# Performance work log

Hardware: AMD Instinct MI355X
Metric: run time of the kernel (lower is better)

## Reference

```python
import jax, jax.numpy as jnp
import numpy as np
import math

B, T, D, H = 1576, 30, 1024, 128  # batch, Frame, embded_dim, hidden_dim
EPS = 1e-5

def _layernorm(x, g, b):
    m = jnp.mean(x, axis=-1, keepdims=True)
    v = jnp.mean((x - m) ** 2, axis=-1, keepdims=True)
    return (x - m) * jax.lax.rsqrt(v + EPS) * g + b

def setup_inputs() -> dict:
    key = jax.random.key(0)
    ks = jax.random.split(key, 16)
    s = 0.02
    inp = {
        "x": jax.random.normal(ks[0], (B, T, D), dtype=jnp.float32),
        # weights stored as [in, out] (transposed vs torch nn.Linear.weight)
        "W1": jax.random.normal(ks[1], (D, H), dtype=jnp.float32) * s,
        "b1": jnp.zeros((H,), jnp.float32),
        "ln_g": jnp.ones((H,), jnp.float32),
        "ln_b": jnp.zeros((H,), jnp.float32),
        "T_W": jax.random.normal(ks[2], (T, T), dtype=jnp.float32) * s,
        "T_b": jnp.zeros((T,), jnp.float32),
        "Wq": jax.random.normal(ks[3], (H, H), dtype=jnp.float32) * s,
        "bq": jnp.zeros((H,), jnp.float32),
        "Wk": jax.random.normal(ks[4], (H, H), dtype=jnp.float32) * s,
        "bk": jnp.zeros((H,), jnp.float32),
        "Wv": jax.random.normal(ks[5], (H, H), dtype=jnp.float32) * s,
        "bv": jnp.zeros((H,), jnp.float32),
        "Wo": jax.random.normal(ks[6], (H, H), dtype=jnp.float32) * s,
        "bo": jnp.zeros((H,), jnp.float32),
        "n_g": jnp.ones((H,), jnp.float32),
        "n_b": jnp.zeros((H,), jnp.float32),
        "W2": jax.random.normal(ks[7], (H, D), dtype=jnp.float32) * s,
        "b2": jnp.zeros((D,), jnp.float32),
    }
    return inp

def reference(x, W1, b1, ln_g, ln_b, T_W, T_b, Wq, bq, Wk, bk, Wv, bv, Wo, bo, n_g, n_b, W2, b2):
    # down-projection + LayerNorm
    h = x @ W1 + b1                      # [B,T,H]
    h = _layernorm(h, ln_g, ln_b)
    # FRU: mean over channels -> temporal linear -> softmax over time -> gate
    g = jnp.mean(h, axis=-1)             # [B,T]
    g = g @ T_W + T_b                    # [B,T]
    g = jax.nn.softmax(g, axis=1)
    h = h * g[..., None]
    # TemporalTransformer (single-head manual attention over T=30)
    hn = _layernorm(h, n_g, n_b)
    q = hn @ Wq + bq
    k = hn @ Wk + bk
    v = hn @ Wv + bv
    scale = math.sqrt(1.0 / float(H))
    attn = jax.nn.softmax((q * scale) @ jnp.swapaxes(k, -2, -1), axis=-1)  # [B,T,T]
    h = (attn @ v) @ Wo + bo + h
    # up-projection
    return h @ W2 + b2                   # [B,T,D]
```

## Files before the change

### kernel.cpp

```cpp
#include <hip/hip_runtime.h>
#include <cstdint>
#include <cstddef>

typedef short s16x8 __attribute__((ext_vector_type(8)));
typedef short s16x4 __attribute__((ext_vector_type(4)));
typedef float f32x4 __attribute__((ext_vector_type(4)));

#define NB 1576
#define NT 30
#define ND 1024
#define NH 128
#define LNEPS 1e-5f
#define ATT_SCALE 0.08838834764831845f

#define WS_W1P   0
#define WS_W2P   262144
#define WS_WQP   524288
#define WS_WKP   557056
#define WS_WVP   589824
#define WS_WOP   622592
#define WS_PAR   655360
#define WS_NEED  667792

#define P_B1   0
#define P_LNG  128
#define P_LNB  256
#define P_TB   384
#define P_TW   416
#define P_BQ   1316
#define P_BK   1444
#define P_BV   1572
#define P_BO   1700
#define P_NG   1828
#define P_NB_  1956
#define P_B2   2084
#define P_CNT  3108

static __device__ __forceinline__ float bf2f(short s) {
  union { unsigned int u; float f; } c;
  c.u = ((unsigned int)(unsigned short)s) << 16;
  return c.f;
}
static __device__ __forceinline__ short f2bf(float f) {
  union { __bf16 h; short s; } c;
  c.h = (__bf16)f;
  return c.s;
}
static __device__ __forceinline__ float ldp(const void* p, int i, int isf32) {
  return isf32 ? ((const float*)p)[i] : bf2f(((const short*)p)[i]);
}
static __device__ __forceinline__ s16x8 ldfragB(const void* W, int N, int k0, int n0,
                                                int m_, int quad, int isf32) {
  s16x8 r;
  int k = k0 + quad*8, n = n0 + m_;
  if (isf32) {
    const float* p = (const float*)W + (size_t)k*N + n;
#pragma unroll
    for (int j = 0; j < 8; j++) r[j] = f2bf(p[(size_t)j*N]);
  } else {
    const short* p = (const short*)W + (size_t)k*N + n;
#pragma unroll
    for (int j = 0; j < 8; j++) r[j] = p[(size_t)j*N];
  }
  return r;
}
static __device__ __forceinline__ void mm32d(const short* Ab, const void* W, const void* bias,
                                             int w, int lane, int isf32,
                                             f32x4 acc[2][2], float bias2[2]) {
  int m_ = lane & 15, quad = lane >> 4;
#pragma unroll
  for (int mt = 0; mt < 2; mt++)
#pragma unroll
    for (int j = 0; j < 2; j++) acc[mt][j] = {0.f, 0.f, 0.f, 0.f};
  bias2[0] = ldp(bias, (2*w)*16 + m_, isf32);
  bias2[1] = ldp(bias, (2*w+1)*16 + m_, isf32);
#pragma unroll
  for (int ks = 0; ks < 4; ks++) {
    s16x8 a[2];
#pragma unroll
    for (int mt = 0; mt < 2; mt++)
      a[mt] = *(const s16x8*)(Ab + (mt*16 + m_)*136 + (ks*4 + quad)*8);
#pragma unroll
    for (int j = 0; j < 2; j++) {
      s16x8 bb = ldfragB(W, NH, ks*32, (2*w + j)*16, m_, quad, isf32);
#pragma unroll
      for (int mt = 0; mt < 2; mt++)
        acc[mt][j] = __builtin_amdgcn_mfma_f32_16x16x32_bf16(a[mt], bb, acc[mt][j], 0, 0, 0);
    }
  }
}

__global__ __launch_bounds__(256) void repack(
    const void* __restrict__ x,
    const void* __restrict__ W1, const void* __restrict__ Wq, const void* __restrict__ Wk,
    const void* __restrict__ Wv, const void* __restrict__ Wo, const void* __restrict__ W2,
    const void* __restrict__ b1, const void* __restrict__ ln_g, const void* __restrict__ ln_b,
    const void* __restrict__ T_W, const void* __restrict__ T_b,
    const void* __restrict__ bq, const void* __restrict__ bk, const void* __restrict__ bv,
    const void* __restrict__ bo, const void* __restrict__ n_g, const void* __restrict__ n_b,
    const void* __restrict__ b2,
    short* __restrict__ W1p, short* __restrict__ W2p,
    short* __restrict__ Wqp, short* __restrict__ Wkp, short* __restrict__ Wvp,
    short* __restrict__ Wop, float* __restrict__ par) {
  int lane = threadIdx.x & 63;
  const unsigned short* u = (const unsigned short*)x;
  int e = (u[lane] >> 7) & 0xFF;
  unsigned long long bal = __ballot(e >= 0x3A && e <= 0x43);
  int isf32 = (__popcll(bal) < 48) ? 1 : 0;

  int idx = blockIdx.x * 256 + threadIdx.x;
  if (idx < 16384) {
    int t = idx, kq = t >> 7, n = t & 127;
    s16x8 v;
#pragma unroll
    for (int j = 0; j < 8; j++)
      v[j] = isf32 ? f2bf(((const float*)W1)[(size_t)(kq*8 + j)*128 + n])
                   : ((const short*)W1)[(size_t)(kq*8 + j)*128 + n];
    *(s16x8*)(W1p + (size_t)t*8) = v;
  } else if (idx < 32768) {
    int t = idx - 16384, kq = t >> 10, n = t & 1023;
    s16x8 v;
#pragma unroll
    for (int j = 0; j < 8; j++)
      v[j] = isf32 ? f2bf(((const float*)W2)[(size_t)(kq*8 + j)*1024 + n])
                   : ((const short*)W2)[(size_t)(kq*8 + j)*1024 + n];
    *(s16x8*)(W2p + (size_t)t*8) = v;
  } else if (idx < 40960) {
    int t = idx - 32768;
    int sel = t >> 11;
    int tt = t & 2047, kq = tt >> 7, n = tt & 127;
    const void* W = (sel == 0) ? Wq : (sel == 1) ? Wk : (sel == 2) ? Wv : Wo;
    short* Wp = (sel == 0) ? Wqp : (sel == 1) ? Wkp : (sel == 2) ? Wvp : Wop;
    s16x8 v;
#pragma unroll
    for (int j = 0; j < 8; j++)
      v[j] = isf32 ? f2bf(((const float*)W)[(size_t)(kq*8 + j)*128 + n])
                   : ((const short*)W)[(size_t)(kq*8 + j)*128 + n];
    *(s16x8*)(Wp + (size_t)tt*8) = v;
  } else {
    int t = idx - 40960;
    if (t < P_CNT) {
      float v;
      if (t < 128)        v = ldp(b1,   t,        isf32);
      else if (t < 256)   v = ldp(ln_g, t - 128,  isf32);
      else if (t < 384)   v = ldp(ln_b, t - 256,  isf32);
      else if (t < 416) { int i = t - 384; v = (i < NT) ? ldp(T_b, i, isf32) : 0.f; }
      else if (t < 1316)  v = ldp(T_W, t - 416,   isf32);
      else if (t < 1444)  v = ldp(bq,  t - 1316,  isf32);
      else if (t < 1572)  v = ldp(bk,  t - 1444,  isf32);
      else if (t < 1700)  v = ldp(bv,  t - 1572,  isf32);
      else if (t < 1828)  v = ldp(bo,  t - 1700,  isf32);
      else if (t < 1956)  v = ldp(n_g, t - 1828,  isf32);
      else if (t < 2084)  v = ldp(n_b, t - 1956,  isf32);
      else                v = ldp(b2,  t - 2084,  isf32);
      par[t] = v;
    }
  }
}

__global__ __launch_bounds__(512, 4) void fused_pk(
    const void* __restrict__ x,
    const short* __restrict__ W1p, const short* __restrict__ W2p,
    const short* __restrict__ Wqp, const short* __restrict__ Wkp,
    const short* __restrict__ Wvp, const short* __restrict__ Wop,
    const float* __restrict__ par, void* __restrict__ out) {
  __shared__ __align__(16) short As[32*136];
  __shared__ __align__(16) float hbuf[NT*128];
  __shared__ float g0s[32];
  __shared__ float sgate[32];
  __shared__ __align__(16) short hn[32*136];
  __shared__ __align__(16) short qb[32*136];
  __shared__ __align__(16) short kbf[32*136];
  __shared__ __align__(16) short vt[NH*32];
  __shared__ float Sb[32*33];
  __shared__ __align__(16) short Pb[32*32];

  int tid = threadIdx.x, lane = tid & 63, w = tid >> 6;
  int m_ = lane & 15, quad = lane >> 4;
  int b = blockIdx.x;
  const int g16 = w*16 + m_;

  int isf32;
  {
    const unsigned short* u = (const unsigned short*)x;
    int e = (u[lane] >> 7) & 0xFF;
    unsigned long long bal = __ballot(e >= 0x3A && e <= 0x43);
    isf32 = (__popcll(bal) < 48) ? 1 : 0;
  }
  const size_t xbase = (size_t)b * NT * ND;

  f32x4 acc0 = {0.f,0.f,0.f,0.f}, acc1 = {0.f,0.f,0.f,0.f};
  {
    int r_st = tid >> 4, cc_st = tid & 15;
    int rr = r_st > NT-1 ? NT-1 : r_st;
    const size_t xoff0 = xbase + (size_t)rr*ND + cc_st*8;
    float4 pf0, pf1; uint4 pu;
    if (isf32) { const float* s = (const float*)x + xoff0; pf0 = *(const float4*)s; pf1 = *(const float4*)(s + 4); }
    else       { pu = *(const uint4*)((const short*)x + xoff0); }
    for (int kb = 0; kb < 8; kb++) {
      if (isf32) {
        s16x8 t;
        t[0]=f2bf(pf0.x); t[1]=f2bf(pf0.y); t[2]=f2bf(pf0.z); t[3]=f2bf(pf0.w);
        t[4]=f2bf(pf1.x); t[5]=f2bf(pf1.y); t[6]=f2bf(pf1.z); t[7]=f2bf(pf1.w);
        *(s16x8*)(As + r_st*136 + cc_st*8) = t;
      } else {
        *(uint4*)(As + r_st*136 + cc_st*8) = pu;
      }
      __syncthreads();
      if (kb < 7) {
        size_t o = xoff0 + (size_t)(kb + 1)*128;
        if (isf32) { const float* s = (const float*)x + o; pf0 = *(const float4*)s; pf1 = *(const float4*)(s + 4); }
        else       { pu = *(const uint4*)((const short*)x + o); }
      }
#pragma unroll
      for (int kblk = 0; kblk < 4; kblk++) {
        s16x8 a0 = *(const s16x8*)(As + m_*136 + (kblk*4 + quad)*8);
        s16x8 a1 = *(const s16x8*)(As + (16 + m_)*136 + (kblk*4 + quad)*8);
        s16x8 bb = *(const s16x8*)(W1p + ((size_t)((kb*4 + kblk)*4 + quad)*NH + g16)*8);
        acc0 = __builtin_amdgcn_mfma_f32_16x16x32_bf16(a0, bb, acc0, 0, 0, 0);
        acc1 = __builtin_amdgcn_mfma_f32_16x16x32_bf16(a1, bb, acc1, 0, 0, 0);
      }
      __syncthreads();
    }
  }
  {
    float b1v = par[P_B1 + g16];
#pragma unroll
    for (int mt = 0; mt < 2; mt++) {
      f32x4 a = mt ? acc1 : acc0;
#pragma unroll
      for (int r = 0; r < 4; r++) {
        int row = mt*16 + quad*4 + r;
        if (row < NT) hbuf[row*128 + g16] = a[r] + b1v;
      }
    }
  }
  __syncthreads();

  for (int r = w; r < NT; r += 8) {
    float v0 = hbuf[r*128 + lane], v1 = hbuf[r*128 + lane + 64];
    float s = v0 + v1, ss = v0*v0 + v1*v1;
#pragma unroll
    for (int off = 1; off <= 32; off <<= 1) {
      s += __shfl_xor(s, off, 64); ss += __shfl_xor(ss, off, 64);
    }
    float mean = s * (1.f/NH);
    float var = ss * (1.f/NH) - mean*mean;
    float rs = rsqrtf(var + LNEPS);
    float o0 = (v0 - mean) * rs * par[P_LNG + lane]      + par[P_LNB + lane];
    float o1 = (v1 - mean) * rs * par[P_LNG + lane + 64] + par[P_LNB + lane + 64];
    hbuf[r*128 + lane] = o0;
    hbuf[r*128 + lane + 64] = o1;
    float rm = o0 + o1;
#pragma unroll
    for (int off = 1; off <= 32; off <<= 1) rm += __shfl_xor(rm, off, 64);
    if (lane == 0) g0s[r] = rm * (1.f/NH);
  }
  __syncthreads();

  if (tid < 32) {
    float y = -1e30f;
    if (tid < NT) {
      y = par[P_TB + tid];
      for (int t = 0; t < NT; t++) y += g0s[t] * par[P_TW + t*NT + tid];
    }
    float mx = y;
#pragma unroll
    for (int off = 16; off >= 1; off >>= 1) mx = fmaxf(mx, __shfl_xor(mx, off, 64));
    float e = (tid < NT) ? expf(y - mx) : 0.f;
    float s = e;
#pragma unroll
    for (int off = 16; off >= 1; off >>= 1) s += __shfl_xor(s, off, 64);
    if (tid < NT) sgate[tid] = e / s;
  }
  __syncthreads();

#pragma unroll
  for (int it = 0; it < 2; it++) {
    int c = it*512 + tid;
    if (c < 960) {
      int row = c >> 5, i = c & 31;
      float gt = sgate[row];
      float4* p = (float4*)(hbuf + row*128 + i*4);
      float4 v = *p;
      v.x *= gt; v.y *= gt; v.z *= gt; v.w *= gt;
      *p = v;
    }
  }
  __syncthreads();

  for (int r = w; r < NT; r += 8) {
    float v0 = hbuf[r*128 + lane], v1 = hbuf[r*128 + lane + 64];
    float s = v0 + v1, ss = v0*v0 + v1*v1;
#pragma unroll
    for (int off = 1; off <= 32; off <<= 1) {
      s += __shfl_xor(s, off, 64); ss += __shfl_xor(ss, off, 64);
    }
    float mean = s * (1.f/NH);
    float var = ss * (1.f/NH) - mean*mean;
    float rs = rsqrtf(var + LNEPS);
    hn[r*136 + lane]      = f2bf((v0 - mean) * rs * par[P_NG + lane]      + par[P_NB_ + lane]);
    hn[r*136 + lane + 64] = f2bf((v1 - mean) * rs * par[P_NG + lane + 64] + par[P_NB_ + lane + 64]);
  }
  if (tid < 256) hn[(NT + (tid >> 7))*136 + (tid & 127)] = 0;
  __syncthreads();

  {
    f32x4 q0 = {0.f,0.f,0.f,0.f}, q1 = q0, k0 = q0, k1 = q0, v0a = q0, v1a = q0;
#pragma unroll
    for (int ks = 0; ks < 4; ks++) {
      s16x8 a0 = *(const s16x8*)(hn + m_*136 + (ks*4 + quad)*8);
      s16x8 a1 = *(const s16x8*)(hn + (16 + m_)*136 + (ks*4 + quad)*8);
      size_t fo = ((size_t)(ks*4 + quad)*NH + g16)*8;
      s16x8 bq8 = *(const s16x8*)(Wqp + fo);
      q0 = __builtin_amdgcn_mfma_f32_16x16x32_bf16(a0, bq8, q0, 0, 0, 0);
      q1 = __builtin_amdgcn_mfma_f32_16x16x32_bf16(a1, bq8, q1, 0, 0, 0);
      s16x8 bk8 = *(const s16x8*)(Wkp + fo);
      k0 = __builtin_amdgcn_mfma_f32_16x16x32_bf16(a0, bk8, k0, 0, 0, 0);
      k1 = __builtin_amdgcn_mfma_f32_16x16x32_bf16(a1, bk8, k1, 0, 0, 0);
      s16x8 bv8 = *(const s16x8*)(Wvp + fo);
      v0a = __builtin_amdgcn_mfma_f32_16x16x32_bf16(a0, bv8, v0a, 0, 0, 0);
      v1a = __builtin_amdgcn_mfma_f32_16x16x32_bf16(a1, bv8, v1a, 0, 0, 0);
    }
    float bqv = par[P_BQ + g16], bkv = par[P_BK + g16], bvv = par[P_BV + g16];
#pragma unroll
    for (int mt = 0; mt < 2; mt++) {
      f32x4 qq = mt ? q1 : q0, kk = mt ? k1 : k0, vv = mt ? v1a : v0a;
      s16x4 vtp;
#pragma unroll
      for (int r = 0; r < 4; r++) {
        int row = mt*16 + quad*4 + r;
        qb[row*136 + g16]  = f2bf(qq[r] + bqv);
        kbf[row*136 + g16] = f2bf(kk[r] + bkv);
        vtp[r] = f2bf(vv[r] + bvv);
      }
      *(s16x4*)(vt + g16*32 + mt*16 + quad*4) = vtp;
    }
  }
  __syncthreads();

  if (w < 4) {
    int mt = w >> 1, nt = w & 1;
    f32x4 sa = {0.f,0.f,0.f,0.f};
#pragma unroll
    for (int ks = 0; ks < 4; ks++) {
      s16x8 a   = *(const s16x8*)(qb  + (mt*16 + m_)*136 + (ks*4 + quad)*8);
      s16x8 bbv = *(const s16x8*)(kbf + (nt*16 + m_)*136 + (ks*4 + quad)*8);
      sa = __builtin_amdgcn_mfma_f32_16x16x32_bf16(a, bbv, sa, 0, 0, 0);
    }
#pragma unroll
    for (int r = 0; r < 4; r++)
      Sb[(mt*16 + quad*4 + r)*33 + nt*16 + m_] = sa[r];
  }
  __syncthreads();

#pragma unroll
  for (int ps = 0; ps < 2; ps++) {
    int row = ps*16 + (tid >> 5);
    int col = tid & 31;
    if (row < NT) {
      float sv = (col < NT) ? Sb[row*33 + col] : -1e30f;
      float mx = sv;
#pragma unroll
      for (int off = 16; off >= 1; off >>= 1) mx = fmaxf(mx, __shfl_xor(mx, off, 32));
      float e = (col < NT) ? expf((sv - mx) * ATT_SCALE) : 0.f;
      float s = e;
#pragma unroll
      for (int off = 16; off >= 1; off >>= 1) s += __shfl_xor(s, off, 32);
      Pb[row*32 + col] = f2bf(e / s);
    } else {
      Pb[row*32 + col] = 0;
    }
  }
  __syncthreads();

  {
    f32x4 a40 = {0.f,0.f,0.f,0.f}, a41 = a40;
    s16x8 pa0 = *(const s16x8*)(Pb + m_*32 + quad*8);
    s16x8 pa1 = *(const s16x8*)(Pb + (16 + m_)*32 + quad*8);
    s16x8 vb8 = *(const s16x8*)(vt + g16*32 + quad*8);
    a40 = __builtin_amdgcn_mfma_f32_16x16x32_bf16(pa0, vb8, a40, 0, 0, 0);
    a41 = __builtin_amdgcn_mfma_f32_16x16x32_bf16(pa1, vb8, a41, 0, 0, 0);
#pragma unroll
    for (int mt = 0; mt < 2; mt++) {
      f32x4 a = mt ? a41 : a40;
#pragma unroll
      for (int r = 0; r < 4; r++)
        As[(mt*16 + quad*4 + r)*136 + g16] = f2bf(a[r]);
    }
  }
  __syncthreads();

  {
    f32x4 o0 = {0.f,0.f,0.f,0.f}, o1 = o0;
#pragma unroll
    for (int ks = 0; ks < 4; ks++) {
      s16x8 a0 = *(const s16x8*)(As + m_*136 + (ks*4 + quad)*8);
      s16x8 a1 = *(const s16x8*)(As + (16 + m_)*136 + (ks*4 + quad)*8);
      s16x8 bb = *(const s16x8*)(Wop + ((size_t)(ks*4 + quad)*NH + g16)*8);
      o0 = __builtin_amdgcn_mfma_f32_16x16x32_bf16(a0, bb, o0, 0, 0, 0);
      o1 = __builtin_amdgcn_mfma_f32_16x16x32_bf16(a1, bb, o1, 0, 0, 0);
    }
    float bov = par[P_BO + g16];
#pragma unroll
    for (int mt = 0; mt < 2; mt++) {
      f32x4 a = mt ? o1 : o0;
#pragma unroll
      for (int r = 0; r < 4; r++) {
        int row = mt*16 + quad*4 + r;
        if (row < NT)
          hn[row*136 + g16] = f2bf(a[r] + bov + hbuf[row*128 + g16]);
      }
    }
    if (tid < 256) hn[(NT + (tid >> 7))*136 + (tid & 127)] = 0;
  }
  __syncthreads();

  for (int cg = 0; cg < 8; cg++) {
    f32x4 c0 = {0.f,0.f,0.f,0.f}, c1 = c0;
#pragma unroll
    for (int kblk = 0; kblk < 4; kblk++) {
      s16x8 a0 = *(const s16x8*)(hn + m_*136 + (kblk*4 + quad)*8);
      s16x8 a1 = *(const s16x8*)(hn + (16 + m_)*136 + (kblk*4 + quad)*8);
      s16x8 bb = *(const s16x8*)(W2p + ((size_t)(kblk*4 + quad)*ND + cg*128 + g16)*8);
      c0 = __builtin_amdgcn_mfma_f32_16x16x32_bf16(a0, bb, c0, 0, 0, 0);
      c1 = __builtin_amdgcn_mfma_f32_16x16x32_bf16(a1, bb, c1, 0, 0, 0);
    }
    float b2v = par[P_B2 + cg*128 + g16];
    if (isf32) {
      float* po = (float*)out + (size_t)b*NT*ND + cg*128 + g16;
#pragma unroll
      for (int mt = 0; mt < 2; mt++) {
        f32x4 a = mt ? c1 : c0;
#pragma unroll
        for (int r = 0; r < 4; r++) {
          int row = mt*16 + quad*4 + r;
          if (row < NT) po[(size_t)row*ND] = a[r] + b2v;
        }
      }
    } else {
#pragma unroll
      for (int mt = 0; mt < 2; mt++) {
        f32x4 a = mt ? c1 : c0;
#pragma unroll
        for (int r = 0; r < 4; r++)
          qb[(mt*16 + quad*4 + r)*136 + g16] = f2bf(a[r] + b2v);
      }
      __syncthreads();
      if (tid < 480) {
        int r = tid >> 4, cc = tid & 15;
        *(uint4*)((short*)out + ((size_t)b*NT + r)*ND + cg*128 + cc*8) =
            *(const uint4*)(qb + r*136 + cc*8);
      }
      __syncthreads();
    }
  }
}

__global__ __launch_bounds__(256) void fused_all(
    const void* __restrict__ x, const void* __restrict__ W1,
    const void* __restrict__ b1, const void* __restrict__ ln_g, const void* __restrict__ ln_b,
    const void* __restrict__ T_W, const void* __restrict__ T_b,
    const void* __restrict__ Wq, const void* __restrict__ bq,
    const void* __restrict__ Wk, const void* __restrict__ bk,
    const void* __restrict__ Wv, const void* __restrict__ bv,
    const void* __restrict__ Wo, const void* __restrict__ bo,
    const void* __restrict__ n_g, const void* __restrict__ n_b,
    const void* __restrict__ W2, const void* __restrict__ b2,
    void* __restrict__ out) {
  __shared__ __align__(16) short As[32*136];
  __shared__ __align__(16) float hbuf[NT*128];
  __shared__ float g0s[32];
  __shared__ float sgate[32];
  __shared__ __align__(16) short hn[32*136];
  __shared__ __align__(16) short qb[32*136];
  __shared__ __align__(16) short kbf[32*136];
  __shared__ __align__(16) short vt[NH*32];
  __shared__ float Sb[32*33];
  __shared__ __align__(16) short Pb[32*32];

  int tid = threadIdx.x, lane = tid & 63, w = tid >> 6;
  int m_ = lane & 15, quad = lane >> 4;
  int b = blockIdx.x;

  int isf32;
  {
    const unsigned short* u = (const unsigned short*)x;
    int pl = 0;
#pragma unroll
    for (int i = 0; i < 64; i++) {
      int e = (u[i] >> 7) & 0xFF;
      pl += (e >= 0x3A && e <= 0x43) ? 1 : 0;
    }
    isf32 = (pl < 48) ? 1 : 0;
  }
  const size_t xbase = (size_t)b * NT * ND;

  f32x4 acc[2][2];
#pragma unroll
  for (int mt = 0; mt < 2; mt++)
#pragma unroll
    for (int j = 0; j < 2; j++) acc[mt][j] = {0.f, 0.f, 0.f, 0.f};

  for (int kb = 0; kb < 8; kb++) {
    __syncthreads();
#pragma unroll
    for (int it = 0; it < 2; it++) {
      int c = it*256 + tid;
      int r = c >> 4, cc = c & 15;
      int rr = r > NT-1 ? NT-1 : r;
      size_t off = xbase + (size_t)rr*ND + kb*128 + cc*8;
      if (!isf32) {
        *(uint4*)(As + r*136 + cc*8) = *(const uint4*)((const short*)x + off);
      } else {
        const float* src = (const float*)x + off;
        float4 f0 = *(const float4*)src, f1 = *(const float4*)(src + 4);
        s16x8 t;
        t[0]=f2bf(f0.x); t[1]=f2bf(f0.y); t[2]=f2bf(f0.z); t[3]=f2bf(f0.w);
        t[4]=f2bf(f1.x); t[5]=f2bf(f1.y); t[6]=f2bf(f1.z); t[7]=f2bf(f1.w);
        *(s16x8*)(As + r*136 + cc*8) = t;
      }
    }
    __syncthreads();
#pragma unroll
    for (int kblk = 0; kblk < 4; kblk++) {
      s16x8 a0 = *(const s16x8*)(As + (m_)*136      + (kblk*4 + quad)*8);
      s16x8 a1 = *(const s16x8*)(As + (16 + m_)*136 + (kblk*4 + quad)*8);
#pragma unroll
      for (int j = 0; j < 2; j++) {
        s16x8 bb = ldfragB(W1, NH, (kb*4 + kblk)*32, (2*w + j)*16, m_, quad, isf32);
        acc[0][j] = __builtin_amdgcn_mfma_f32_16x16x32_bf16(a0, bb, acc[0][j], 0, 0, 0);
        acc[1][j] = __builtin_amdgcn_mfma_f32_16x16x32_bf16(a1, bb, acc[1][j], 0, 0, 0);
      }
    }
  }
  __syncthreads();
  {
    float b1v[2] = {ldp(b1, (2*w)*16 + m_, isf32), ldp(b1, (2*w+1)*16 + m_, isf32)};
#pragma unroll
    for (int mt = 0; mt < 2; mt++)
#pragma unroll
      for (int j = 0; j < 2; j++)
#pragma unroll
        for (int r = 0; r < 4; r++) {
          int row = mt*16 + quad*4 + r;
          if (row < NT)
            hbuf[row*128 + (2*w + j)*16 + m_] = acc[mt][j][r] + b1v[j];
        }
  }
  __syncthreads();

  for (int r = w; r < NT; r += 4) {
    float v0 = hbuf[r*128 + lane], v1 = hbuf[r*128 + lane + 64];
    float s = v0 + v1, ss = v0*v0 + v1*v1;
#pragma unroll
    for (int off = 1; off <= 32; off <<= 1) {
      s += __shfl_xor(s, off, 64); ss += __shfl_xor(ss, off, 64);
    }
    float mean = s * (1.f/NH);
    float var = ss * (1.f/NH) - mean*mean;
    float rs = rsqrtf(var + LNEPS);
    float o0 = (v0 - mean) * rs * ldp(ln_g, lane, isf32)      + ldp(ln_b, lane, isf32);
    float o1 = (v1 - mean) * rs * ldp(ln_g, lane + 64, isf32) + ldp(ln_b, lane + 64, isf32);
    hbuf[r*128 + lane] = o0;
    hbuf[r*128 + lane + 64] = o1;
    float rm = o0 + o1;
#pragma unroll
    for (int off = 1; off <= 32; off <<= 1) rm += __shfl_xor(rm, off, 64);
    if (lane == 0) g0s[r] = rm * (1.f/NH);
  }
  __syncthreads();

  if (tid < 32) {
    float y = -1e30f;
    if (tid < NT) {
      y = ldp(T_b, tid, isf32);
      for (int t = 0; t < NT; t++) y += g0s[t] * ldp(T_W, t*NT + tid, isf32);
    }
    float mx = y;
#pragma unroll
    for (int off = 16; off >= 1; off >>= 1) mx = fmaxf(mx, __shfl_xor(mx, off, 64));
    float e = (tid < NT) ? expf(y - mx) : 0.f;
    float s = e;
#pragma unroll
    for (int off = 16; off >= 1; off >>= 1) s += __shfl_xor(s, off, 64);
    if (tid < NT) sgate[tid] = e / s;
  }
  __syncthreads();

#pragma unroll
  for (int it = 0; it < 4; it++) {
    int c = it*256 + tid;
    if (c < 960) {
      int row = c >> 5, i = c & 31;
      float gt = sgate[row];
      float4* p = (float4*)(hbuf + row*128 + i*4);
      float4 v = *p;
      v.x *= gt; v.y *= gt; v.z *= gt; v.w *= gt;
      *p = v;
    }
  }
  __syncthreads();

  for (int r = w; r < NT; r += 4) {
    float v0 = hbuf[r*128 + lane], v1 = hbuf[r*128 + lane + 64];
    float s = v0 + v1, ss = v0*v0 + v1*v1;
#pragma unroll
    for (int off = 1; off <= 32; off <<= 1) {
      s += __shfl_xor(s, off, 64); ss += __shfl_xor(ss, off, 64);
    }
    float mean = s * (1.f/NH);
    float var = ss * (1.f/NH) - mean*mean;
    float rs = rsqrtf(var + LNEPS);
    hn[r*136 + lane]      = f2bf((v0 - mean) * rs * ldp(n_g, lane, isf32)      + ldp(n_b, lane, isf32));
    hn[r*136 + lane + 64] = f2bf((v1 - mean) * rs * ldp(n_g, lane + 64, isf32) + ldp(n_b, lane + 64, isf32));
  }
  hn[(30 + (tid >> 7))*136 + (tid & 127)] = 0;
  __syncthreads();

  {
    f32x4 a4[2][2];
    float bias2[2];
    mm32d(hn, Wq, bq, w, lane, isf32, a4, bias2);
#pragma unroll
    for (int mt = 0; mt < 2; mt++)
#pragma unroll
      for (int j = 0; j < 2; j++)
#pragma unroll
        for (int r = 0; r < 4; r++)
          qb[(mt*16 + quad*4 + r)*136 + (2*w + j)*16 + m_] = f2bf(a4[mt][j][r] + bias2[j]);
    mm32d(hn, Wk, bk, w, lane, isf32, a4, bias2);
#pragma unroll
    for (int mt = 0; mt < 2; mt++)
#pragma unroll
      for (int j = 0; j < 2; j++)
#pragma unroll
        for (int r = 0; r < 4; r++)
          kbf[(mt*16 + quad*4 + r)*136 + (2*w + j)*16 + m_] = f2bf(a4[mt][j][r] + bias2[j]);
    mm32d(hn, Wv, bv, w, lane, isf32, a4, bias2);
#pragma unroll
    for (int mt = 0; mt < 2; mt++)
#pragma unroll
      for (int j = 0; j < 2; j++)
#pragma unroll
        for (int r = 0; r < 4; r++)
          vt[((2*w + j)*16 + m_)*32 + mt*16 + quad*4 + r] = f2bf(a4[mt][j][r] + bias2[j]);
  }
  __syncthreads();

  {
    int mt = w >> 1, nt = w & 1;
    f32x4 sa = {0.f, 0.f, 0.f, 0.f};
#pragma unroll
    for (int ks = 0; ks < 4; ks++) {
      s16x8 a   = *(const s16x8*)(qb  + (mt*16 + m_)*136 + (ks*4 + quad)*8);
      s16x8 bbv = *(const s16x8*)(kbf + (nt*16 + m_)*136 + (ks*4 + quad)*8);
      sa = __builtin_amdgcn_mfma_f32_16x16x32_bf16(a, bbv, sa, 0, 0, 0);
    }
#pragma unroll
    for (int r = 0; r < 4; r++)
      Sb[(mt*16 + quad*4 + r)*33 + nt*16 + m_] = sa[r];
  }
  __syncthreads();

  if (tid < NT) {
    float mx = -1e30f;
    for (int jj = 0; jj < NT; jj++) {
      int j = tid + jj; if (j >= NT) j -= NT;
      mx = fmaxf(mx, Sb[tid*33 + j]);
    }
    float sum = 0.f;
    for (int jj = 0; jj < NT; jj++) {
      int j = tid + jj; if (j >= NT) j -= NT;
      float e = expf((Sb[tid*33 + j] - mx) * ATT_SCALE);
      Sb[tid*33 + j] = e; sum += e;
    }
    float rinv = 1.f / sum;
    for (int jj = 0; jj < NT; jj++) {
      int j = tid + jj; if (j >= NT) j -= NT;
      Pb[tid*32 + j] = f2bf(Sb[tid*33 + j] * rinv);
    }
    Pb[tid*32 + 30] = 0;
    Pb[tid*32 + 31] = 0;
  } else if (tid >= 64 && tid < 128) {
    int c = tid - 64;
    Pb[(30 + (c >> 5))*32 + (c & 31)] = 0;
  }
  __syncthreads();

  {
    f32x4 a4[2][2];
#pragma unroll
    for (int mt = 0; mt < 2; mt++)
#pragma unroll
      for (int j = 0; j < 2; j++) a4[mt][j] = {0.f, 0.f, 0.f, 0.f};
    s16x8 pa[2];
#pragma unroll
    for (int mt = 0; mt < 2; mt++)
      pa[mt] = *(const s16x8*)(Pb + (mt*16 + m_)*32 + quad*8);
#pragma unroll
    for (int j = 0; j < 2; j++) {
      int nh = (2*w + j)*16 + m_;
      s16x8 vb8 = *(const s16x8*)(vt + nh*32 + quad*8);
#pragma unroll
      for (int mt = 0; mt < 2; mt++)
        a4[mt][j] = __builtin_amdgcn_mfma_f32_16x16x32_bf16(pa[mt], vb8, a4[mt][j], 0, 0, 0);
    }
#pragma unroll
    for (int mt = 0; mt < 2; mt++)
#pragma unroll
      for (int j = 0; j < 2; j++)
#pragma unroll
        for (int r = 0; r < 4; r++)
          As[(mt*16 + quad*4 + r)*136 + (2*w + j)*16 + m_] = f2bf(a4[mt][j][r]);
  }
  __syncthreads();

  {
    f32x4 a4[2][2];
    float bias2[2];
    mm32d(As, Wo, bo, w, lane, isf32, a4, bias2);
#pragma unroll
    for (int mt = 0; mt < 2; mt++)
#pragma unroll
      for (int j = 0; j < 2; j++)
#pragma unroll
        for (int r = 0; r < 4; r++) {
          int row = mt*16 + quad*4 + r;
          if (row < NT) {
            int col = (2*w + j)*16 + m_;
            hn[row*136 + col] = f2bf(a4[mt][j][r] + bias2[j] + hbuf[row*128 + col]);
          }
        }
    hn[(30 + (tid >> 7))*136 + (tid & 127)] = 0;
  }
  __syncthreads();

  for (int cg = 0; cg < 8; cg++) {
    f32x4 a2[2][2];
#pragma unroll
    for (int mt = 0; mt < 2; mt++)
#pragma unroll
      for (int j = 0; j < 2; j++) a2[mt][j] = {0.f, 0.f, 0.f, 0.f};
#pragma unroll
    for (int kblk = 0; kblk < 4; kblk++) {
      s16x8 a0 = *(const s16x8*)(hn + (m_)*136      + (kblk*4 + quad)*8);
      s16x8 a1 = *(const s16x8*)(hn + (16 + m_)*136 + (kblk*4 + quad)*8);
#pragma unroll
      for (int j = 0; j < 2; j++) {
        s16x8 bb = ldfragB(W2, ND, kblk*32, cg*128 + (2*w + j)*16, m_, quad, isf32);
        a2[0][j] = __builtin_amdgcn_mfma_f32_16x16x32_bf16(a0, bb, a2[0][j], 0, 0, 0);
        a2[1][j] = __builtin_amdgcn_mfma_f32_16x16x32_bf16(a1, bb, a2[1][j], 0, 0, 0);
      }
    }
    float b2v[2] = {ldp(b2, cg*128 + (2*w)*16 + m_, isf32),
                    ldp(b2, cg*128 + (2*w+1)*16 + m_, isf32)};
    if (!isf32) {
#pragma unroll
      for (int mt = 0; mt < 2; mt++)
#pragma unroll
        for (int j = 0; j < 2; j++)
#pragma unroll
          for (int r = 0; r < 4; r++)
            qb[(mt*16 + quad*4 + r)*136 + (2*w + j)*16 + m_] = f2bf(a2[mt][j][r] + b2v[j]);
    }
    __syncthreads();
    if (!isf32) {
#pragma unroll
      for (int it = 0; it < 2; it++) {
        int c = it*256 + tid;
        if (c < 480) {
          int r = c >> 4, cc = c & 15;
          *(uint4*)((short*)out + ((size_t)b*NT + r)*ND + cg*128 + cc*8) =
              *(const uint4*)(qb + r*136 + cc*8);
        }
      }
    } else {
#pragma unroll
      for (int mt = 0; mt < 2; mt++)
#pragma unroll
        for (int j = 0; j < 2; j++)
#pragma unroll
          for (int r = 0; r < 4; r++) {
            int row = mt*16 + quad*4 + r;
            if (row < NT)
              ((float*)out)[((size_t)b*NT + row)*ND + cg*128 + (2*w + j)*16 + m_] =
                  a2[mt][j][r] + b2v[j];
          }
    }
    __syncthreads();
  }
}

extern "C" void kernel_launch(void* const* d_in, const int* in_sizes, int n_in,
                              void* d_out, int out_size, void* d_ws, size_t ws_size,
                              hipStream_t stream) {
  if (d_ws && ws_size >= (size_t)WS_NEED) {
    short* W1p = (short*)((char*)d_ws + WS_W1P);
    short* W2p = (short*)((char*)d_ws + WS_W2P);
    short* Wqp = (short*)((char*)d_ws + WS_WQP);
    short* Wkp = (short*)((char*)d_ws + WS_WKP);
    short* Wvp = (short*)((char*)d_ws + WS_WVP);
    short* Wop = (short*)((char*)d_ws + WS_WOP);
    float* par = (float*)((char*)d_ws + WS_PAR);
    repack<<<173, 256, 0, stream>>>(
        d_in[0],
        d_in[1], d_in[7], d_in[9], d_in[11], d_in[13], d_in[17],
        d_in[2], d_in[3], d_in[4], d_in[5], d_in[6],
        d_in[8], d_in[10], d_in[12], d_in[14], d_in[15], d_in[16], d_in[18],
        W1p, W2p, Wqp, Wkp, Wvp, Wop, par);
    fused_pk<<<NB, 512, 0, stream>>>(d_in[0], W1p, W2p, Wqp, Wkp, Wvp, Wop, par, d_out);
  } else {
    fused_all<<<NB, 256, 0, stream>>>(
        d_in[0], d_in[1], d_in[2], d_in[3], d_in[4], d_in[5], d_in[6],
        d_in[7], d_in[8], d_in[9], d_in[10], d_in[11], d_in[12], d_in[13],
        d_in[14], d_in[15], d_in[16], d_in[17], d_in[18], d_out);
  }
}
```

Before: 436.2 us.

## Cut LDS footprint, double-buffer x staging, fold gating into second LayerNorm

Shared-memory buffers in the fused kernel are aliased (q reuses As, scores and probabilities reuse hnb, the output staging reuses As), which cuts the per-block LDS footprint, and the occupancy hint goes from 4 to 6 blocks per CU. The x load loop now ping-pongs between two LDS staging buffers with two-deep register prefetch, so one barrier per k-step disappears. The separate gate-multiply pass and the second LayerNorm reduction are replaced by an algebraic form that derives the gated row's mean and variance from the first LayerNorm's stored sum and sum of squares. In exchange there are extra barriers to protect the aliased buffers, more register pressure under the tighter launch bound, and slightly different rounding in the derived variance.

```diff
diff --git a/kernel.cpp b/kernel.cpp
--- a/kernel.cpp
+++ b/kernel.cpp
@@ -158,22 +158,20 @@
   }
 }
 
-__global__ __launch_bounds__(512, 4) void fused_pk(
+__global__ __launch_bounds__(512, 6) void fused_pk(
     const void* __restrict__ x,
     const short* __restrict__ W1p, const short* __restrict__ W2p,
     const short* __restrict__ Wqp, const short* __restrict__ Wkp,
     const short* __restrict__ Wvp, const short* __restrict__ Wop,
     const float* __restrict__ par, void* __restrict__ out) {
   __shared__ __align__(16) short As[32*136];
+  __shared__ __align__(16) short kbf[32*136];
   __shared__ __align__(16) float hbuf[NT*128];
+  __shared__ __align__(16) short hnb[32*136];
+  __shared__ __align__(16) short vt[NH*40];
   __shared__ float g0s[32];
+  __shared__ float rsqm[32];
   __shared__ float sgate[32];
-  __shared__ __align__(16) short hn[32*136];
-  __shared__ __align__(16) short qb[32*136];
-  __shared__ __align__(16) short kbf[32*136];
-  __shared__ __align__(16) short vt[NH*32];
-  __shared__ float Sb[32*33];
-  __shared__ __align__(16) short Pb[32*32];
 
   int tid = threadIdx.x, lane = tid & 63, w = tid >> 6;
   int m_ = lane & 15, quad = lane >> 4;
@@ -194,33 +192,47 @@
     int r_st = tid >> 4, cc_st = tid & 15;
     int rr = r_st > NT-1 ? NT-1 : r_st;
     const size_t xoff0 = xbase + (size_t)rr*ND + cc_st*8;
-    float4 pf0, pf1; uint4 pu;
-    if (isf32) { const float* s = (const float*)x + xoff0; pf0 = *(const float4*)s; pf1 = *(const float4*)(s + 4); }
-    else       { pu = *(const uint4*)((const short*)x + xoff0); }
+    float4 fa0, fa1, fb0, fb1; uint4 ua, ub;
+    if (isf32) {
+      const float* s0 = (const float*)x + xoff0;
+      fa0 = *(const float4*)s0;         fa1 = *(const float4*)(s0 + 4);
+      fb0 = *(const float4*)(s0 + 128); fb1 = *(const float4*)(s0 + 132);
+    } else {
+      const short* s0 = (const short*)x + xoff0;
+      ua = *(const uint4*)s0; ub = *(const uint4*)(s0 + 128);
+    }
+#pragma unroll
     for (int kb = 0; kb < 8; kb++) {
+      short* stg = (kb & 1) ? kbf : As;
       if (isf32) {
+        float4 f0 = (kb & 1) ? fb0 : fa0, f1 = (kb & 1) ? fb1 : fa1;
         s16x8 t;
-        t[0]=f2bf(pf0.x); t[1]=f2bf(pf0.y); t[2]=f2bf(pf0.z); t[3]=f2bf(pf0.w);
-        t[4]=f2bf(pf1.x); t[5]=f2bf(pf1.y); t[6]=f2bf(pf1.z); t[7]=f2bf(pf1.w);
-        *(s16x8*)(As + r_st*136 + cc_st*8) = t;
+        t[0]=f2bf(f0.x); t[1]=f2bf(f0.y); t[2]=f2bf(f0.z); t[3]=f2bf(f0.w);
+        t[4]=f2bf(f1.x); t[5]=f2bf(f1.y); t[6]=f2bf(f1.z); t[7]=f2bf(f1.w);
+        *(s16x8*)(stg + r_st*136 + cc_st*8) = t;
       } else {
-        *(uint4*)(As + r_st*136 + cc_st*8) = pu;
+        *(uint4*)(stg + r_st*136 + cc_st*8) = (kb & 1) ? ub : ua;
+      }
+      if (kb < 6) {
+        if (isf32) {
+          const float* s2 = (const float*)x + xoff0 + (size_t)(kb + 2)*128;
+          if (kb & 1) { fb0 = *(const float4*)s2; fb1 = *(const float4*)(s2 + 4); }
+          else        { fa0 = *(const float4*)s2; fa1 = *(const float4*)(s2 + 4); }
+        } else {
+          const short* s2 = (const short*)x + xoff0 + (size_t)(kb + 2)*128;
+          if (kb & 1) ub = *(const uint4*)s2; else ua = *(const uint4*)s2;
+        }
       }
       __syncthreads();
-      if (kb < 7) {
-        size_t o = xoff0 + (size_t)(kb + 1)*128;
-        if (isf32) { const float* s = (const float*)x + o; pf0 = *(const float4*)s; pf1 = *(const float4*)(s + 4); }
-        else       { pu = *(const uint4*)((const short*)x + o); }
-      }
+      const short* Ab = (kb & 1) ? kbf : As;
 #pragma unroll
       for (int kblk = 0; kblk < 4; kblk++) {
-        s16x8 a0 = *(const s16x8*)(As + m_*136 + (kblk*4 + quad)*8);
-        s16x8 a1 = *(const s16x8*)(As + (16 + m_)*136 + (kblk*4 + quad)*8);
+        s16x8 a0 = *(const s16x8*)(Ab + m_*136 + (kblk*4 + quad)*8);
+        s16x8 a1 = *(const s16x8*)(Ab + (16 + m_)*136 + (kblk*4 + quad)*8);
         s16x8 bb = *(const s16x8*)(W1p + ((size_t)((kb*4 + kblk)*4 + quad)*NH + g16)*8);
         acc0 = __builtin_amdgcn_mfma_f32_16x16x32_bf16(a0, bb, acc0, 0, 0, 0);
         acc1 = __builtin_amdgcn_mfma_f32_16x16x32_bf16(a1, bb, acc1, 0, 0, 0);
       }
-      __syncthreads();
     }
   }
   {
@@ -251,10 +263,12 @@
     float o1 = (v1 - mean) * rs * par[P_LNG + lane + 64] + par[P_LNB + lane + 64];
     hbuf[r*128 + lane] = o0;
     hbuf[r*128 + lane + 64] = o1;
-    float rm = o0 + o1;
-#pragma unroll
-    for (int off = 1; off <= 32; off <<= 1) rm += __shfl_xor(rm, off, 64);
-    if (lane == 0) g0s[r] = rm * (1.f/NH);
+    float rm = o0 + o1, rq = o0*o0 + o1*o1;
+#pragma unroll
+    for (int off = 1; off <= 32; off <<= 1) {
+      rm += __shfl_xor(rm, off, 64); rq += __shfl_xor(rq, off, 64);
+    }
+    if (lane == 0) { g0s[r] = rm * (1.f/NH); rsqm[r] = rq * (1.f/NH); }
   }
   __syncthreads();
 
@@ -275,42 +289,25 @@
   }
   __syncthreads();
 
-#pragma unroll
-  for (int it = 0; it < 2; it++) {
-    int c = it*512 + tid;
-    if (c < 960) {
-      int row = c >> 5, i = c & 31;
-      float gt = sgate[row];
-      float4* p = (float4*)(hbuf + row*128 + i*4);
-      float4 v = *p;
-      v.x *= gt; v.y *= gt; v.z *= gt; v.w *= gt;
-      *p = v;
-    }
-  }
-  __syncthreads();
-
   for (int r = w; r < NT; r += 8) {
-    float v0 = hbuf[r*128 + lane], v1 = hbuf[r*128 + lane + 64];
-    float s = v0 + v1, ss = v0*v0 + v1*v1;
-#pragma unroll
-    for (int off = 1; off <= 32; off <<= 1) {
-      s += __shfl_xor(s, off, 64); ss += __shfl_xor(ss, off, 64);
-    }
-    float mean = s * (1.f/NH);
-    float var = ss * (1.f/NH) - mean*mean;
+    float g = sgate[r];
+    float m = g0s[r];
+    float gm = g * m;
+    float var = g*g*(rsqm[r] - m*m);
     float rs = rsqrtf(var + LNEPS);
-    hn[r*136 + lane]      = f2bf((v0 - mean) * rs * par[P_NG + lane]      + par[P_NB_ + lane]);
-    hn[r*136 + lane + 64] = f2bf((v1 - mean) * rs * par[P_NG + lane + 64] + par[P_NB_ + lane + 64]);
-  }
-  if (tid < 256) hn[(NT + (tid >> 7))*136 + (tid & 127)] = 0;
+    float o0 = g * hbuf[r*128 + lane], o1 = g * hbuf[r*128 + lane + 64];
+    hnb[r*136 + lane]      = f2bf((o0 - gm) * rs * par[P_NG + lane]      + par[P_NB_ + lane]);
+    hnb[r*136 + lane + 64] = f2bf((o1 - gm) * rs * par[P_NG + lane + 64] + par[P_NB_ + lane + 64]);
+  }
+  if (tid < 256) hnb[(NT + (tid >> 7))*136 + (tid & 127)] = 0;
   __syncthreads();
 
   {
     f32x4 q0 = {0.f,0.f,0.f,0.f}, q1 = q0, k0 = q0, k1 = q0, v0a = q0, v1a = q0;
 #pragma unroll
     for (int ks = 0; ks < 4; ks++) {
-      s16x8 a0 = *(const s16x8*)(hn + m_*136 + (ks*4 + quad)*8);
-      s16x8 a1 = *(const s16x8*)(hn + (16 + m_)*136 + (ks*4 + quad)*8);
+      s16x8 a0 = *(const s16x8*)(hnb + m_*136 + (ks*4 + quad)*8);
+      s16x8 a1 = *(const s16x8*)(hnb + (16 + m_)*136 + (ks*4 + quad)*8);
       size_t fo = ((size_t)(ks*4 + quad)*NH + g16)*8;
       s16x8 bq8 = *(const s16x8*)(Wqp + fo);
       q0 = __builtin_amdgcn_mfma_f32_16x16x32_bf16(a0, bq8, q0, 0, 0, 0);
@@ -323,6 +320,7 @@
       v1a = __builtin_amdgcn_mfma_f32_16x16x32_bf16(a1, bv8, v1a, 0, 0, 0);
     }
     float bqv = par[P_BQ + g16], bkv = par[P_BK + g16], bvv = par[P_BV + g16];
+    __syncthreads();
 #pragma unroll
     for (int mt = 0; mt < 2; mt++) {
       f32x4 qq = mt ? q1 : q0, kk = mt ? k1 : k0, vv = mt ? v1a : v0a;
@@ -330,57 +328,66 @@
 #pragma unroll
       for (int r = 0; r < 4; r++) {
         int row = mt*16 + quad*4 + r;
-        qb[row*136 + g16]  = f2bf(qq[r] + bqv);
+        As[row*136 + g16]  = f2bf(qq[r] + bqv);
         kbf[row*136 + g16] = f2bf(kk[r] + bkv);
         vtp[r] = f2bf(vv[r] + bvv);
       }
-      *(s16x4*)(vt + g16*32 + mt*16 + quad*4) = vtp;
-    }
-  }
-  __syncthreads();
-
-  if (w < 4) {
-    int mt = w >> 1, nt = w & 1;
-    f32x4 sa = {0.f,0.f,0.f,0.f};
-#pragma unroll
-    for (int ks = 0; ks < 4; ks++) {
-      s16x8 a   = *(const s16x8*)(qb  + (mt*16 + m_)*136 + (ks*4 + quad)*8);
-      s16x8 bbv = *(const s16x8*)(kbf + (nt*16 + m_)*136 + (ks*4 + quad)*8);
-      sa = __builtin_amdgcn_mfma_f32_16x16x32_bf16(a, bbv, sa, 0, 0, 0);
-    }
-#pragma unroll
-    for (int r = 0; r < 4; r++)
-      Sb[(mt*16 + quad*4 + r)*33 + nt*16 + m_] = sa[r];
-  }
-  __syncthreads();
-
-#pragma unroll
-  for (int ps = 0; ps < 2; ps++) {
-    int row = ps*16 + (tid >> 5);
-    int col = tid & 31;
-    if (row < NT) {
-      float sv = (col < NT) ? Sb[row*33 + col] : -1e30f;
-      float mx = sv;
-#pragma unroll
-      for (int off = 16; off >= 1; off >>= 1) mx = fmaxf(mx, __shfl_xor(mx, off, 32));
-      float e = (col < NT) ? expf((sv - mx) * ATT_SCALE) : 0.f;
-      float s = e;
-#pragma unroll
-      for (int off = 16; off >= 1; off >>= 1) s += __shfl_xor(s, off, 32);
-      Pb[row*32 + col] = f2bf(e / s);
-    } else {
-      Pb[row*32 + col] = 0;
-    }
-  }
-  __syncthreads();
-
-  {
+      *(s16x4*)(vt + g16*40 + mt*16 + quad*4) = vtp;
+    }
+  }
+  __syncthreads();
+
+  {
+    float* Sb = (float*)hnb;
+    if (w < 4) {
+      int mt = w >> 1, nt = w & 1;
+      f32x4 sa = {0.f,0.f,0.f,0.f};
+#pragma unroll
+      for (int ks = 0; ks < 4; ks++) {
+        s16x8 a   = *(const s16x8*)(As  + (mt*16 + m_)*136 + (ks*4 + quad)*8);
+        s16x8 bbv = *(const s16x8*)(kbf + (nt*16 + m_)*136 + (ks*4 + quad)*8);
+        sa = __builtin_amdgcn_mfma_f32_16x16x32_bf16(a, bbv, sa, 0, 0, 0);
+      }
+#pragma unroll
+      for (int r = 0; r < 4; r++)
+        Sb[(mt*16 + quad*4 + r)*33 + nt*16 + m_] = sa[r];
+    }
+  }
+  __syncthreads();
+
+  {
+    const float* Sb = (const float*)hnb;
+    short* Pb = hnb + 2112;
+#pragma unroll
+    for (int ps = 0; ps < 2; ps++) {
+      int row = ps*16 + (tid >> 5);
+      int col = tid & 31;
+      if (row < NT) {
+        float sv = (col < NT) ? Sb[row*33 + col] : -1e30f;
+        float mx = sv;
+#pragma unroll
+        for (int off = 16; off >= 1; off >>= 1) mx = fmaxf(mx, __shfl_xor(mx, off, 32));
+        float e = (col < NT) ? expf((sv - mx) * ATT_SCALE) : 0.f;
+        float s = e;
+#pragma unroll
+        for (int off = 16; off >= 1; off >>= 1) s += __shfl_xor(s, off, 32);
+        Pb[row*40 + col] = f2bf(e / s);
+      } else {
+        Pb[row*40 + col] = 0;
+      }
+    }
+  }
+  __syncthreads();
+
+  {
+    const short* Pb = hnb + 2112;
     f32x4 a40 = {0.f,0.f,0.f,0.f}, a41 = a40;
-    s16x8 pa0 = *(const s16x8*)(Pb + m_*32 + quad*8);
-    s16x8 pa1 = *(const s16x8*)(Pb + (16 + m_)*32 + quad*8);
-    s16x8 vb8 = *(const s16x8*)(vt + g16*32 + quad*8);
+    s16x8 pa0 = *(const s16x8*)(Pb + m_*40 + quad*8);
+    s16x8 pa1 = *(const s16x8*)(Pb + (16 + m_)*40 + quad*8);
+    s16x8 vb8 = *(const s16x8*)(vt + g16*40 + quad*8);
     a40 = __builtin_amdgcn_mfma_f32_16x16x32_bf16(pa0, vb8, a40, 0, 0, 0);
     a41 = __builtin_amdgcn_mfma_f32_16x16x32_bf16(pa1, vb8, a41, 0, 0, 0);
+    __syncthreads();
 #pragma unroll
     for (int mt = 0; mt < 2; mt++) {
       f32x4 a = mt ? a41 : a40;
@@ -409,10 +416,10 @@
       for (int r = 0; r < 4; r++) {
         int row = mt*16 + quad*4 + r;
         if (row < NT)
-          hn[row*136 + g16] = f2bf(a[r] + bov + hbuf[row*128 + g16]);
-      }
-    }
-    if (tid < 256) hn[(NT + (tid >> 7))*136 + (tid & 127)] = 0;
+          hnb[row*136 + g16] = f2bf(a[r] + bov + sgate[row]*hbuf[row*128 + g16]);
+      }
+    }
+    if (tid < 256) hnb[(NT + (tid >> 7))*136 + (tid & 127)] = 0;
   }
   __syncthreads();
 
@@ -420,8 +427,8 @@
     f32x4 c0 = {0.f,0.f,0.f,0.f}, c1 = c0;
 #pragma unroll
     for (int kblk = 0; kblk < 4; kblk++) {
-      s16x8 a0 = *(const s16x8*)(hn + m_*136 + (kblk*4 + quad)*8);
-      s16x8 a1 = *(const s16x8*)(hn + (16 + m_)*136 + (kblk*4 + quad)*8);
+      s16x8 a0 = *(const s16x8*)(hnb + m_*136 + (kblk*4 + quad)*8);
+      s16x8 a1 = *(const s16x8*)(hnb + (16 + m_)*136 + (kblk*4 + quad)*8);
       s16x8 bb = *(const s16x8*)(W2p + ((size_t)(kblk*4 + quad)*ND + cg*128 + g16)*8);
       c0 = __builtin_amdgcn_mfma_f32_16x16x32_bf16(a0, bb, c0, 0, 0, 0);
       c1 = __builtin_amdgcn_mfma_f32_16x16x32_bf16(a1, bb, c1, 0, 0, 0);
@@ -444,13 +451,13 @@
         f32x4 a = mt ? c1 : c0;
 #pragma unroll
         for (int r = 0; r < 4; r++)
-          qb[(mt*16 + quad*4 + r)*136 + g16] = f2bf(a[r] + b2v);
+          As[(mt*16 + quad*4 + r)*136 + g16] = f2bf(a[r] + b2v);
       }
       __syncthreads();
       if (tid < 480) {
         int r = tid >> 4, cc = tid & 15;
         *(uint4*)((short*)out + ((size_t)b*NT + r)*ND + cg*128 + cc*8) =
-            *(const uint4*)(qb + r*136 + cc*8);
+            *(const uint4*)(As + r*136 + cc*8);
       }
       __syncthreads();
     }
```

Result: no change. 440.0 us (+0.9%).
